# Optimization experiments

Hardware: AMD Instinct MI355X
Metric: run time of the kernel (lower is better)

## Reference

```python
import jax, jax.numpy as jnp
import numpy as np

S, D, P, R, E, M, K = 1024, 1024, 2816, 64, 8, 16, 1


def setup_inputs() -> dict:
    key = jax.random.key(0)
    ks = jax.random.split(key, 10)
    xav_a = (2.0 / (P + R)) ** 0.5   # xavier_uniform-like std for adapters
    xav_d = (2.0 / (D + P)) ** 0.5   # xavier for down projections
    bank_s = (1.0 / D) ** 0.5        # keep basis columns O(1)
    return {
        "hidden_states": jax.random.normal(ks[0], (S, D), jnp.float32),
        "expert_indices": jax.random.randint(ks[1], (S, K), 0, E),
        "expert_weights": jax.random.uniform(ks[2], (S, K), jnp.float32),
        "up_adapters": jax.random.normal(ks[3], (E, P, R), jnp.float32) * xav_a,
        "gate_adapters": jax.random.normal(ks[4], (E, P, R), jnp.float32) * xav_a,
        "up_mixture_logits": jax.random.normal(ks[5], (E, M), jnp.float32) * 0.01,
        "gate_mixture_logits": jax.random.normal(ks[6], (E, M), jnp.float32) * 0.01,
        "down_projections": jax.random.normal(ks[7], (E, D, P), jnp.float32) * xav_d,
        "up_bank": jax.random.normal(ks[8], (M, D, R), jnp.float32) * bank_s,
        "gate_bank": jax.random.normal(ks[9], (M, D, R), jnp.float32) * bank_s,
    }


def reference(hidden_states, expert_indices, expert_weights,
              up_adapters, gate_adapters, up_mixture_logits,
              gate_mixture_logits, down_projections, up_bank, gate_bank):
    n_experts = down_projections.shape[0]
    # SparseMixer: token-independent mixture weights over global bases (softmax)
    alpha_up = jax.nn.softmax(up_mixture_logits, axis=-1)      # [E, M]
    alpha_gate = jax.nn.softmax(gate_mixture_logits, axis=-1)  # [E, M]
    # Compose per-expert mixed bases: sum_j alpha_{e,j} B_j -> [E, D, R]
    up_mixed = jnp.einsum('em,mdr->edr', alpha_up, up_bank)
    gate_mixed = jnp.einsum('em,mdr->edr', alpha_gate, gate_bank)
    # Recomposed Up/Gate weights: A_e @ mixed_e^T -> [E, P, D]
    W_up = jnp.einsum('epr,edr->epd', up_adapters, up_mixed)
    W_gate = jnp.einsum('epr,edr->epd', gate_adapters, gate_mixed)
    # Combine routing weights per (token, expert): sum over topk slots
    onehot = (expert_indices[..., None] == jnp.arange(n_experts)).astype(hidden_states.dtype)  # [S,K,E]
    comb = jnp.einsum('ske,sk->se', onehot, expert_weights)  # [S, E]
    out = jnp.zeros_like(hidden_states)
    for e in range(n_experts):  # fixed small expert count
        up = hidden_states @ W_up[e].T        # [S, P]
        gate = hidden_states @ W_gate[e].T    # [S, P]
        inter = jax.nn.silu(gate) * up        # gated activation
        out = out + (inter @ down_projections[e].T) * comb[:, e:e + 1]
    return out
```

## Files before the change

### kernel.cpp

```cpp
#include <hip/hip_runtime.h>
#include <hip/hip_bf16.h>
#include <math.h>

#define S 1024
#define D 1024
#define P 2816
#define R 64
#define E 8
#define M 16
#define KSPLIT 4
#define KQ (P / KSPLIT)
#define NIT (KQ / 64)
#define ZT 16
#define ACH ((E * P * R) / 8)

typedef __attribute__((ext_vector_type(8))) short short8;
typedef __attribute__((ext_vector_type(4))) float floatx4;

static __device__ inline unsigned short f2bf(float f) {
  __hip_bfloat16 h = __float2bfloat16(f);
  return *reinterpret_cast<unsigned short*>(&h);
}
static __device__ inline short8 pack8(float4 a, float4 b) {
  short8 v;
  v[0] = f2bf(a.x); v[1] = f2bf(a.y); v[2] = f2bf(a.z); v[3] = f2bf(a.w);
  v[4] = f2bf(b.x); v[5] = f2bf(b.y); v[6] = f2bf(b.z); v[7] = f2bf(b.w);
  return v;
}

__global__ __launch_bounds__(256) void k_pre(
    const float* __restrict__ up_logits, const float* __restrict__ gate_logits,
    const float* __restrict__ up_bank, const float* __restrict__ gate_bank,
    const float* __restrict__ H, const float* __restrict__ Aup,
    const float* __restrict__ Agate, const int* __restrict__ idx,
    unsigned short* __restrict__ Hbf, unsigned short* __restrict__ mxT,
    unsigned short* __restrict__ Aubf, unsigned short* __restrict__ Agbf,
    int* __restrict__ perm, int* __restrict__ offs,
    float* __restrict__ tbuf, float* __restrict__ out) {
  int b = blockIdx.x, t = threadIdx.x;
  int g = b * 256 + t;
  float4 z4 = make_float4(0.f, 0.f, 0.f, 0.f);
#pragma unroll
  for (int j = 0; j < 4; ++j)
    *(float4*)(out + (size_t)b * 4096 + j * 1024 + t * 4) = z4;
  *(float2*)(tbuf + (size_t)g * 2) = make_float2(0.f, 0.f);

  if (b == 0) {
    __shared__ int hist[E];
    __shared__ int basearr[E];
    if (t < E) hist[t] = 0;
    __syncthreads();
    int e4[4];
#pragma unroll
    for (int j = 0; j < 4; ++j) {
      e4[j] = idx[t + j * 256];
      atomicAdd(&hist[e4[j]], 1);
    }
    __syncthreads();
    if (t == 0) {
      int run = 0;
      for (int i = 0; i < E; ++i) { basearr[i] = run; offs[i] = run; run += hist[i]; }
      offs[E] = S;
    }
    __syncthreads();
#pragma unroll
    for (int j = 0; j < 4; ++j) {
      int pos = atomicAdd(&basearr[e4[j]], 1);
      perm[pos] = t + j * 256;
    }
  }

  {
    const float* hs = H + (size_t)g * 16;
    float4 h0 = *(const float4*)hs, h1 = *(const float4*)(hs + 4);
    float4 h2 = *(const float4*)(hs + 8), h3 = *(const float4*)(hs + 12);
    *(short8*)(Hbf + (size_t)g * 16) = pack8(h0, h1);
    *(short8*)(Hbf + (size_t)g * 16 + 8) = pack8(h2, h3);
  }
#pragma unroll
  for (int j = 0; j < 3; ++j) {
    int c = g + j * 65536;
    if (c < ACH) {
      const float* su = Aup + (size_t)c * 8;
      const float* sg = Agate + (size_t)c * 8;
      float4 u0 = *(const float4*)su, u1 = *(const float4*)(su + 4);
      float4 g0 = *(const float4*)sg, g1 = *(const float4*)(sg + 4);
      *(short8*)(Aubf + (size_t)c * 8) = pack8(u0, u1);
      *(short8*)(Agbf + (size_t)c * 8) = pack8(g0, g1);
    }
  }

  __shared__ float alpha[2][E][M];
  if (t < 16) {
    int mat = t >> 3, e = t & 7;
    const float* lg = (mat ? gate_logits : up_logits) + e * M;
    float v[M], mx = -1e30f, s = 0.f;
#pragma unroll
    for (int m = 0; m < M; ++m) { v[m] = lg[m]; mx = fmaxf(mx, v[m]); }
#pragma unroll
    for (int m = 0; m < M; ++m) { v[m] = expf(v[m] - mx); s += v[m]; }
#pragma unroll
    for (int m = 0; m < M; ++m) alpha[mat][e][m] = v[m] / s;
  }
  __syncthreads();
  int d = g >> 6, r = g & 63;
  float au[E] = {0, 0, 0, 0, 0, 0, 0, 0}, ag[E] = {0, 0, 0, 0, 0, 0, 0, 0};
#pragma unroll
  for (int m = 0; m < M; ++m) {
    float vu = up_bank[((size_t)m * D + d) * R + r];
    float vg = gate_bank[((size_t)m * D + d) * R + r];
#pragma unroll
    for (int e = 0; e < E; ++e) {
      au[e] += alpha[0][e][m] * vu;
      ag[e] += alpha[1][e][m] * vg;
    }
  }
#pragma unroll
  for (int e = 0; e < E; ++e) {
    mxT[((size_t)e * 128 + r) * D + d] = f2bf(au[e]);
    mxT[((size_t)e * 128 + 64 + r) * D + d] = f2bf(ag[e]);
  }
}

__global__ __launch_bounds__(256) void k_t(
    const unsigned short* __restrict__ Hbf, const unsigned short* __restrict__ mxT,
    const int* __restrict__ perm, const int* __restrict__ offs,
    float* __restrict__ tbuf) {
  int e = blockIdx.x;
  int end = offs[e + 1];
  int t = threadIdx.x, lane = t & 63, w = t >> 6;
  int quad = lane >> 4, l15 = lane & 15;
  int row0 = offs[e] + blockIdx.y * 64 + w * 16;
  if (row0 >= end) return;
  int k0 = blockIdx.z * (D / ZT);
  int pos = row0 + l15;
  int tok = (pos < end) ? perm[pos] : -1;
  const unsigned short* hrow = Hbf + (size_t)(tok < 0 ? 0 : tok) * D + k0;
  floatx4 acc[8];
#pragma unroll
  for (int nt = 0; nt < 8; ++nt) acc[nt] = (floatx4){0.f, 0.f, 0.f, 0.f};
#pragma unroll
  for (int ks = 0; ks < 2; ++ks) {
    int kc = ks * 32 + quad * 8;
    short8 a = (short8){0, 0, 0, 0, 0, 0, 0, 0};
    if (tok >= 0) a = *(const short8*)(hrow + kc);
#pragma unroll
    for (int nt = 0; nt < 8; ++nt) {
      short8 bb = *(const short8*)(mxT + ((size_t)e * 128 + nt * 16 + l15) * D + k0 + kc);
      acc[nt] = __builtin_amdgcn_mfma_f32_16x16x32_bf16(a, bb, acc[nt], 0, 0, 0);
    }
  }
#pragma unroll
  for (int reg = 0; reg < 4; ++reg) {
    int p = row0 + quad * 4 + reg;
    if (p < end) {
#pragma unroll
      for (int nt = 0; nt < 8; ++nt)
        atomicAdd(&tbuf[(size_t)p * 128 + nt * 16 + l15], acc[nt][reg]);
    }
  }
}

__global__ __launch_bounds__(256) void k_inter(
    const float* __restrict__ tbuf, const unsigned short* __restrict__ Aubf,
    const unsigned short* __restrict__ Agbf, const int* __restrict__ offs,
    unsigned short* __restrict__ inter) {
  int e = blockIdx.x;
  int start = offs[e] + blockIdx.y * 16;
  int end = offs[e + 1];
  if (start >= end) return;
  int t = threadIdx.x, lane = t & 63, w = t >> 6;
  int quad = lane >> 4, l15 = lane & 15;
  int p0 = blockIdx.z * 256 + w * 64;
  int pos = start + l15;
  bool okA = pos < end;
  floatx4 accu[4], accg[4];
#pragma unroll
  for (int nt = 0; nt < 4; ++nt) {
    accu[nt] = (floatx4){0.f, 0.f, 0.f, 0.f};
    accg[nt] = (floatx4){0.f, 0.f, 0.f, 0.f};
  }
#pragma unroll
  for (int ks = 0; ks < 2; ++ks) {
    int kc = ks * 32 + quad * 8;
    short8 au = (short8){0, 0, 0, 0, 0, 0, 0, 0};
    short8 ag = (short8){0, 0, 0, 0, 0, 0, 0, 0};
    if (okA) {
      const float* tp = tbuf + (size_t)pos * 128 + kc;
      au = pack8(*(const float4*)tp, *(const float4*)(tp + 4));
      ag = pack8(*(const float4*)(tp + 64), *(const float4*)(tp + 68));
    }
#pragma unroll
    for (int nt = 0; nt < 4; ++nt) {
      size_t prow = (size_t)e * P + p0 + nt * 16 + l15;
      short8 bu = *(const short8*)(Aubf + prow * R + kc);
      short8 bg = *(const short8*)(Agbf + prow * R + kc);
      accu[nt] = __builtin_amdgcn_mfma_f32_16x16x32_bf16(au, bu, accu[nt], 0, 0, 0);
      accg[nt] = __builtin_amdgcn_mfma_f32_16x16x32_bf16(ag, bg, accg[nt], 0, 0, 0);
    }
  }
#pragma unroll
  for (int nt = 0; nt < 4; ++nt)
#pragma unroll
    for (int reg = 0; reg < 4; ++reg) {
      int prow = start + quad * 4 + reg;
      if (prow < end) {
        float gv = accg[nt][reg], uv = accu[nt][reg];
        float val = uv * (gv / (1.f + __expf(-gv)));
        inter[(size_t)prow * P + p0 + nt * 16 + l15] = f2bf(val);
      }
    }
}

__global__ __launch_bounds__(256) void k_down(
    const unsigned short* __restrict__ inter, const float* __restrict__ Wd,
    const int* __restrict__ perm, const int* __restrict__ offs,
    const float* __restrict__ wts, float* __restrict__ out) {
  int e = blockIdx.x;
  int start = offs[e] + blockIdx.y * 64;
  int end = offs[e + 1];
  if (start >= end) return;
  int kz = blockIdx.z >> 4;
  int d0 = (blockIdx.z & 15) * 64;
  __shared__ unsigned short As[64][72];
  __shared__ unsigned short Bs[64][72];
  int t = threadIdx.x;
  int lane = t & 63, w = t >> 6, quad = lane >> 4, l15 = lane & 15;

  int arow = t >> 2;
  int apos = start + arow;
  bool aok = apos < end;
  const unsigned short* aptr =
      inter + (size_t)(aok ? apos : start) * P + kz * KQ + (t & 3) * 16;
  const float* bptr = Wd + ((size_t)(e * D + d0 + (t >> 2)) * P + kz * KQ + (t & 3) * 16);

  short8 pa0 = (short8){0, 0, 0, 0, 0, 0, 0, 0}, pa1 = pa0;
  float4 pb[4];
  if (aok) { pa0 = *(const short8*)aptr; pa1 = *(const short8*)(aptr + 8); }
#pragma unroll
  for (int q = 0; q < 4; ++q) pb[q] = *(const float4*)(bptr + q * 4);

  floatx4 acc[4];
#pragma unroll
  for (int dt = 0; dt < 4; ++dt) acc[dt] = (floatx4){0.f, 0.f, 0.f, 0.f};

  for (int it = 0; it < NIT; ++it) {
    *(short8*)&As[arow][(t & 3) * 16] = pa0;
    *(short8*)&As[arow][(t & 3) * 16 + 8] = pa1;
    *(short8*)&Bs[t >> 2][(t & 3) * 16] = pack8(pb[0], pb[1]);
    *(short8*)&Bs[t >> 2][(t & 3) * 16 + 8] = pack8(pb[2], pb[3]);
    __syncthreads();
    if (it + 1 < NIT) {
      int k0 = (it + 1) * 64;
      if (aok) { pa0 = *(const short8*)(aptr + k0); pa1 = *(const short8*)(aptr + k0 + 8); }
#pragma unroll
      for (int q = 0; q < 4; ++q) pb[q] = *(const float4*)(bptr + k0 + q * 4);
    }
#pragma unroll
    for (int ks = 0; ks < 2; ++ks) {
      int kc = ks * 32 + quad * 8;
      short8 a = *(const short8*)&As[w * 16 + l15][kc];
#pragma unroll
      for (int dt = 0; dt < 4; ++dt) {
        short8 b = *(const short8*)&Bs[dt * 16 + l15][kc];
        acc[dt] = __builtin_amdgcn_mfma_f32_16x16x32_bf16(a, b, acc[dt], 0, 0, 0);
      }
    }
    __syncthreads();
  }
#pragma unroll
  for (int reg = 0; reg < 4; ++reg) {
    int pos = start + w * 16 + quad * 4 + reg;
    if (pos < end) {
      int tok = perm[pos];
      float wt = wts[tok];
#pragma unroll
      for (int dt = 0; dt < 4; ++dt)
        atomicAdd(&out[(size_t)tok * D + d0 + dt * 16 + l15], acc[dt][reg] * wt);
    }
  }
}

extern "C" void kernel_launch(void* const* d_in, const int* in_sizes, int n_in,
                              void* d_out, int out_size, void* d_ws, size_t ws_size,
                              hipStream_t stream) {
  const float* H = (const float*)d_in[0];
  const int* idx = (const int*)d_in[1];
  const float* wts = (const float*)d_in[2];
  const float* Aup = (const float*)d_in[3];
  const float* Agate = (const float*)d_in[4];
  const float* upl = (const float*)d_in[5];
  const float* gatel = (const float*)d_in[6];
  const float* Wd = (const float*)d_in[7];
  const float* upb = (const float*)d_in[8];
  const float* gateb = (const float*)d_in[9];
  float* out = (float*)d_out;

  char* ws = (char*)d_ws;
  unsigned short* Hbf = (unsigned short*)ws;
  unsigned short* mxT = Hbf + (size_t)S * D;
  unsigned short* Aubf = mxT + (size_t)E * 128 * D;
  unsigned short* Agbf = Aubf + (size_t)E * P * R;
  unsigned short* inter = Agbf + (size_t)E * P * R;
  float* tbuf = (float*)(inter + (size_t)S * P);
  int* perm = (int*)(tbuf + (size_t)S * 128);
  int* offs = perm + S;

  k_pre<<<256, 256, 0, stream>>>(upl, gatel, upb, gateb, H, Aup, Agate, idx,
                                 Hbf, mxT, Aubf, Agbf, perm, offs, tbuf, out);
  k_t<<<dim3(E, 4, ZT), 256, 0, stream>>>(Hbf, mxT, perm, offs, tbuf);
  k_inter<<<dim3(E, 16, P / 256), 256, 0, stream>>>(tbuf, Aubf, Agbf, offs, inter);
  k_down<<<dim3(E, 4, KSPLIT * 16), 256, 0, stream>>>(inter, Wd, perm, offs, wts, out);
}
```

Measured before the change: 259.5 us.

## Drop split-K and atomics in projection kernels, store bf16 intermediate

Removes the K-split from both the token-by-basis projection kernel and the down-projection kernel, so each block walks the full reduction and writes results with plain stores instead of atomicAdd. The zero-initialisation of the output and intermediate buffer is no longer needed. The intermediate t buffer is now stored as bf16, so the next kernel reads bf16 directly instead of packing fp32. The down kernel now uses 128-row tiles, each wave doing a 2x4 MFMA tile. The grids also cover up to all tokens per expert. The cost is far fewer active blocks with much longer serial K loops, which may underuse the GPU, especially in the bandwidth-heavy down projection.

```diff
diff --git a/kernel.cpp b/kernel.cpp
--- a/kernel.cpp
+++ b/kernel.cpp
@@ -8,10 +8,7 @@
 #define R 64
 #define E 8
 #define M 16
-#define KSPLIT 4
-#define KQ (P / KSPLIT)
-#define NIT (KQ / 64)
-#define ZT 16
+#define NITD (P / 64)
 #define ACH ((E * P * R) / 8)
 
 typedef __attribute__((ext_vector_type(8))) short short8;
@@ -35,15 +32,9 @@
     const float* __restrict__ Agate, const int* __restrict__ idx,
     unsigned short* __restrict__ Hbf, unsigned short* __restrict__ mxT,
     unsigned short* __restrict__ Aubf, unsigned short* __restrict__ Agbf,
-    int* __restrict__ perm, int* __restrict__ offs,
-    float* __restrict__ tbuf, float* __restrict__ out) {
+    int* __restrict__ perm, int* __restrict__ offs) {
   int b = blockIdx.x, t = threadIdx.x;
   int g = b * 256 + t;
-  float4 z4 = make_float4(0.f, 0.f, 0.f, 0.f);
-#pragma unroll
-  for (int j = 0; j < 4; ++j)
-    *(float4*)(out + (size_t)b * 4096 + j * 1024 + t * 4) = z4;
-  *(float2*)(tbuf + (size_t)g * 2) = make_float2(0.f, 0.f);
 
   if (b == 0) {
     __shared__ int hist[E];
@@ -125,29 +116,31 @@
 __global__ __launch_bounds__(256) void k_t(
     const unsigned short* __restrict__ Hbf, const unsigned short* __restrict__ mxT,
     const int* __restrict__ perm, const int* __restrict__ offs,
-    float* __restrict__ tbuf) {
+    unsigned short* __restrict__ tbuf) {
   int e = blockIdx.x;
   int end = offs[e + 1];
   int t = threadIdx.x, lane = t & 63, w = t >> 6;
   int quad = lane >> 4, l15 = lane & 15;
   int row0 = offs[e] + blockIdx.y * 64 + w * 16;
   if (row0 >= end) return;
-  int k0 = blockIdx.z * (D / ZT);
   int pos = row0 + l15;
   int tok = (pos < end) ? perm[pos] : -1;
-  const unsigned short* hrow = Hbf + (size_t)(tok < 0 ? 0 : tok) * D + k0;
+  const unsigned short* hrow = Hbf + (size_t)(tok < 0 ? 0 : tok) * D;
+  const unsigned short* brow = mxT + (size_t)e * 128 * D;
   floatx4 acc[8];
 #pragma unroll
   for (int nt = 0; nt < 8; ++nt) acc[nt] = (floatx4){0.f, 0.f, 0.f, 0.f};
-#pragma unroll
-  for (int ks = 0; ks < 2; ++ks) {
-    int kc = ks * 32 + quad * 8;
-    short8 a = (short8){0, 0, 0, 0, 0, 0, 0, 0};
-    if (tok >= 0) a = *(const short8*)(hrow + kc);
-#pragma unroll
-    for (int nt = 0; nt < 8; ++nt) {
-      short8 bb = *(const short8*)(mxT + ((size_t)e * 128 + nt * 16 + l15) * D + k0 + kc);
-      acc[nt] = __builtin_amdgcn_mfma_f32_16x16x32_bf16(a, bb, acc[nt], 0, 0, 0);
+  for (int kt = 0; kt < 16; ++kt) {
+#pragma unroll
+    for (int ks = 0; ks < 2; ++ks) {
+      int kc = kt * 64 + ks * 32 + quad * 8;
+      short8 a = (short8){0, 0, 0, 0, 0, 0, 0, 0};
+      if (tok >= 0) a = *(const short8*)(hrow + kc);
+#pragma unroll
+      for (int nt = 0; nt < 8; ++nt) {
+        short8 bb = *(const short8*)(brow + (size_t)(nt * 16 + l15) * D + kc);
+        acc[nt] = __builtin_amdgcn_mfma_f32_16x16x32_bf16(a, bb, acc[nt], 0, 0, 0);
+      }
     }
   }
 #pragma unroll
@@ -156,13 +149,13 @@
     if (p < end) {
 #pragma unroll
       for (int nt = 0; nt < 8; ++nt)
-        atomicAdd(&tbuf[(size_t)p * 128 + nt * 16 + l15], acc[nt][reg]);
+        tbuf[(size_t)p * 128 + nt * 16 + l15] = f2bf(acc[nt][reg]);
     }
   }
 }
 
 __global__ __launch_bounds__(256) void k_inter(
-    const float* __restrict__ tbuf, const unsigned short* __restrict__ Aubf,
+    const unsigned short* __restrict__ tbuf, const unsigned short* __restrict__ Aubf,
     const unsigned short* __restrict__ Agbf, const int* __restrict__ offs,
     unsigned short* __restrict__ inter) {
   int e = blockIdx.x;
@@ -186,9 +179,8 @@
     short8 au = (short8){0, 0, 0, 0, 0, 0, 0, 0};
     short8 ag = (short8){0, 0, 0, 0, 0, 0, 0, 0};
     if (okA) {
-      const float* tp = tbuf + (size_t)pos * 128 + kc;
-      au = pack8(*(const float4*)tp, *(const float4*)(tp + 4));
-      ag = pack8(*(const float4*)(tp + 64), *(const float4*)(tp + 68));
+      au = *(const short8*)(tbuf + (size_t)pos * 128 + kc);
+      ag = *(const short8*)(tbuf + (size_t)pos * 128 + 64 + kc);
     }
 #pragma unroll
     for (int nt = 0; nt < 4; ++nt) {
@@ -217,68 +209,80 @@
     const int* __restrict__ perm, const int* __restrict__ offs,
     const float* __restrict__ wts, float* __restrict__ out) {
   int e = blockIdx.x;
-  int start = offs[e] + blockIdx.y * 64;
+  int start = offs[e] + blockIdx.y * 128;
   int end = offs[e + 1];
   if (start >= end) return;
-  int kz = blockIdx.z >> 4;
-  int d0 = (blockIdx.z & 15) * 64;
-  __shared__ unsigned short As[64][72];
+  int d0 = blockIdx.z * 64;
+  __shared__ unsigned short As[128][72];
   __shared__ unsigned short Bs[64][72];
   int t = threadIdx.x;
   int lane = t & 63, w = t >> 6, quad = lane >> 4, l15 = lane & 15;
 
-  int arow = t >> 2;
+  int arow = t >> 1;
   int apos = start + arow;
   bool aok = apos < end;
   const unsigned short* aptr =
-      inter + (size_t)(aok ? apos : start) * P + kz * KQ + (t & 3) * 16;
-  const float* bptr = Wd + ((size_t)(e * D + d0 + (t >> 2)) * P + kz * KQ + (t & 3) * 16);
-
-  short8 pa0 = (short8){0, 0, 0, 0, 0, 0, 0, 0}, pa1 = pa0;
+      inter + (size_t)(aok ? apos : start) * P + (t & 1) * 32;
+  const float* bptr = Wd + ((size_t)(e * D + d0 + (t >> 2)) * P + (t & 3) * 16);
+
+  short8 pa[4];
   float4 pb[4];
-  if (aok) { pa0 = *(const short8*)aptr; pa1 = *(const short8*)(aptr + 8); }
+#pragma unroll
+  for (int q = 0; q < 4; ++q)
+    pa[q] = aok ? *(const short8*)(aptr + q * 8) : (short8){0, 0, 0, 0, 0, 0, 0, 0};
 #pragma unroll
   for (int q = 0; q < 4; ++q) pb[q] = *(const float4*)(bptr + q * 4);
 
-  floatx4 acc[4];
-#pragma unroll
-  for (int dt = 0; dt < 4; ++dt) acc[dt] = (floatx4){0.f, 0.f, 0.f, 0.f};
-
-  for (int it = 0; it < NIT; ++it) {
-    *(short8*)&As[arow][(t & 3) * 16] = pa0;
-    *(short8*)&As[arow][(t & 3) * 16 + 8] = pa1;
+  floatx4 acc[2][4];
+#pragma unroll
+  for (int tt = 0; tt < 2; ++tt)
+#pragma unroll
+    for (int dt = 0; dt < 4; ++dt) acc[tt][dt] = (floatx4){0.f, 0.f, 0.f, 0.f};
+
+  for (int it = 0; it < NITD; ++it) {
+#pragma unroll
+    for (int q = 0; q < 4; ++q)
+      *(short8*)&As[arow][(t & 1) * 32 + q * 8] = pa[q];
     *(short8*)&Bs[t >> 2][(t & 3) * 16] = pack8(pb[0], pb[1]);
     *(short8*)&Bs[t >> 2][(t & 3) * 16 + 8] = pack8(pb[2], pb[3]);
     __syncthreads();
-    if (it + 1 < NIT) {
+    if (it + 1 < NITD) {
       int k0 = (it + 1) * 64;
-      if (aok) { pa0 = *(const short8*)(aptr + k0); pa1 = *(const short8*)(aptr + k0 + 8); }
+#pragma unroll
+      for (int q = 0; q < 4; ++q)
+        pa[q] = aok ? *(const short8*)(aptr + k0 + q * 8) : (short8){0, 0, 0, 0, 0, 0, 0, 0};
 #pragma unroll
       for (int q = 0; q < 4; ++q) pb[q] = *(const float4*)(bptr + k0 + q * 4);
     }
 #pragma unroll
     for (int ks = 0; ks < 2; ++ks) {
       int kc = ks * 32 + quad * 8;
-      short8 a = *(const short8*)&As[w * 16 + l15][kc];
-#pragma unroll
-      for (int dt = 0; dt < 4; ++dt) {
-        short8 b = *(const short8*)&Bs[dt * 16 + l15][kc];
-        acc[dt] = __builtin_amdgcn_mfma_f32_16x16x32_bf16(a, b, acc[dt], 0, 0, 0);
+      short8 a[2], b[4];
+#pragma unroll
+      for (int tt = 0; tt < 2; ++tt) a[tt] = *(const short8*)&As[w * 32 + tt * 16 + l15][kc];
+#pragma unroll
+      for (int dt = 0; dt < 4; ++dt) b[dt] = *(const short8*)&Bs[dt * 16 + l15][kc];
+#pragma unroll
+      for (int tt = 0; tt < 2; ++tt)
+#pragma unroll
+        for (int dt = 0; dt < 4; ++dt)
+          acc[tt][dt] = __builtin_amdgcn_mfma_f32_16x16x32_bf16(a[tt], b[dt], acc[tt][dt], 0, 0, 0);
+    }
+    __syncthreads();
+  }
+#pragma unroll
+  for (int tt = 0; tt < 2; ++tt)
+#pragma unroll
+    for (int reg = 0; reg < 4; ++reg) {
+      int pos = start + w * 32 + tt * 16 + quad * 4 + reg;
+      if (pos < end) {
+        int tok = perm[pos];
+        float wt = wts[tok];
+#pragma unroll
+        for (int dt = 0; dt < 4; ++dt)
+          out[(size_t)tok * D + d0 + dt * 16 + l15] = acc[tt][dt][reg] * wt;
       }
     }
-    __syncthreads();
-  }
-#pragma unroll
-  for (int reg = 0; reg < 4; ++reg) {
-    int pos = start + w * 16 + quad * 4 + reg;
-    if (pos < end) {
-      int tok = perm[pos];
-      float wt = wts[tok];
-#pragma unroll
-      for (int dt = 0; dt < 4; ++dt)
-        atomicAdd(&out[(size_t)tok * D + d0 + dt * 16 + l15], acc[dt][reg] * wt);
-    }
-  }
 }
 
 extern "C" void kernel_launch(void* const* d_in, const int* in_sizes, int n_in,
@@ -302,13 +306,13 @@
   unsigned short* Aubf = mxT + (size_t)E * 128 * D;
   unsigned short* Agbf = Aubf + (size_t)E * P * R;
   unsigned short* inter = Agbf + (size_t)E * P * R;
-  float* tbuf = (float*)(inter + (size_t)S * P);
+  unsigned short* tbuf = inter + (size_t)S * P;
   int* perm = (int*)(tbuf + (size_t)S * 128);
   int* offs = perm + S;
 
   k_pre<<<256, 256, 0, stream>>>(upl, gatel, upb, gateb, H, Aup, Agate, idx,
-                                 Hbf, mxT, Aubf, Agbf, perm, offs, tbuf, out);
-  k_t<<<dim3(E, 4, ZT), 256, 0, stream>>>(Hbf, mxT, perm, offs, tbuf);
-  k_inter<<<dim3(E, 16, P / 256), 256, 0, stream>>>(tbuf, Aubf, Agbf, offs, inter);
-  k_down<<<dim3(E, 4, KSPLIT * 16), 256, 0, stream>>>(inter, Wd, perm, offs, wts, out);
-}
+                                 Hbf, mxT, Aubf, Agbf, perm, offs);
+  k_t<<<dim3(E, 16), 256, 0, stream>>>(Hbf, mxT, perm, offs, tbuf);
+  k_inter<<<dim3(E, 64, P / 256), 256, 0, stream>>>(tbuf, Aubf, Agbf, offs, inter);
+  k_down<<<dim3(E, 8, 16), 256, 0, stream>>>(inter, Wd, perm, offs, wts, out);
+}
```

Result: slower. 396.1 us (+52.7%).
